# Optimization experiments

Hardware: AMD Instinct MI355X
Metric: run time of the kernel (lower is better)

The kernel has to match this reference:

```python
import jax, jax.numpy as jnp
import numpy as np
from jax import lax

T, IN_DIM, H = 8192, 512, 1024


def setup_inputs() -> dict:
    key = jax.random.key(0)
    ks = jax.random.split(key, 6)
    def lin(k, fan_in, shape):
        return jax.random.normal(k, shape, dtype=jnp.float32) / np.sqrt(fan_in)
    return {
        "x": jax.random.normal(ks[0], (T, IN_DIM), dtype=jnp.float32),
        "W_ih_0": lin(ks[1], IN_DIM, (IN_DIM, 4 * H)),
        "W_hh_0": lin(ks[2], H, (H, 4 * H)),
        "b_0": jnp.zeros((4 * H,), dtype=jnp.float32),
        "W_ih_1": lin(ks[3], H, (H, 4 * H)),
        "W_hh_1": lin(ks[4], H, (H, 4 * H)),
        "b_1": jnp.zeros((4 * H,), dtype=jnp.float32),
    }


def _lstm_layer(inp, W_ih, W_hh, b):
    """inp: (T, D) -> hiddens (T, H). Input projection batched across all T."""
    hdim = W_hh.shape[0]
    xg = inp @ W_ih  # (T, 4H), all-timestep GEMM

    def step(carry, xg_t):
        h, c = carry
        gates = xg_t + h @ W_hh + b  # (4H,)
        i, f, g, o = jnp.split(gates, 4, axis=-1)
        i = jax.nn.sigmoid(i)
        f = jax.nn.sigmoid(f)
        g = jnp.tanh(g)
        o = jax.nn.sigmoid(o)
        new_c = f * c + i * g
        new_h = o * jnp.tanh(new_c)
        return (new_h, new_c), new_h

    init = (jnp.zeros((hdim,), inp.dtype), jnp.zeros((hdim,), inp.dtype))
    _, hiddens = lax.scan(step, init, xg)
    return hiddens  # (T, H)


def reference(x, W_ih_0, W_hh_0, b_0, W_ih_1, W_hh_1, b_1):
    h1 = _lstm_layer(x, W_ih_0, W_hh_0, b_0)
    h2 = _lstm_layer(h1, W_ih_1, W_hh_1, b_1)
    return h2
```

## Files before the change

### kernel.cpp

```cpp
#include <hip/hip_runtime.h>
#include <stdint.h>


#define TT    8192
#define INDIM 512
#define HH    1024
#define G4    4096
#define NBLK  256

#define SENT 0x7FC00000u

typedef float f32x4 __attribute__((ext_vector_type(4)));

__device__ __forceinline__ float sigf(float x) { return 1.0f / (1.0f + __expf(-x)); }

__global__ void fill4_kernel(float* __restrict__ p, long n4, uint32_t pat) {
  float pv = __uint_as_float(pat);
  f32x4 v = { pv, pv, pv, pv };
  long i = (long)blockIdx.x * blockDim.x + threadIdx.x;
  long stride = (long)gridDim.x * blockDim.x;
  for (; i < n4; i += stride) {
    const float* a = p + i * 4;
    asm volatile("global_store_dwordx4 %0, %1, off sc0 sc1" :: "v"(a), "v"(v) : "memory");
  }
}

__global__ __launch_bounds__(256, 2) void gemm_bias_f32(
    const float* __restrict__ A, const float* __restrict__ B,
    const float* __restrict__ bias, float* __restrict__ C,
    int M, int N, int K)
{
  constexpr int BM = 128, BN = 128, BK = 16, TM = 8, TN = 8;
  __shared__ float As[BK][BM];
  __shared__ float Bs[BK][BN];
  const int tid = threadIdx.x;
  const int bm = blockIdx.y * BM;
  const int bn = blockIdx.x * BN;
  const int tm = (tid >> 4) * TM;
  const int tn = (tid & 15) * TN;
  float acc[TM][TN] = {};
  for (int k0 = 0; k0 < K; k0 += BK) {
    #pragma unroll
    for (int i = 0; i < 2; ++i) {
      int idx = tid * 2 + i;
      int r = idx >> 2, c4 = idx & 3;
      float4 a = *(const float4*)(A + (size_t)(bm + r) * K + k0 + c4 * 4);
      As[c4 * 4 + 0][r] = a.x;
      As[c4 * 4 + 1][r] = a.y;
      As[c4 * 4 + 2][r] = a.z;
      As[c4 * 4 + 3][r] = a.w;
    }
    #pragma unroll
    for (int i = 0; i < 2; ++i) {
      int idx = tid * 2 + i;
      int r = idx >> 5, c4 = idx & 31;
      *(float4*)&Bs[r][c4 * 4] = *(const float4*)(B + (size_t)(k0 + r) * N + bn + c4 * 4);
    }
    __syncthreads();
    #pragma unroll
    for (int kk = 0; kk < BK; ++kk) {
      float ar[TM], br[TN];
      *(float4*)&ar[0] = *(const float4*)&As[kk][tm];
      *(float4*)&ar[4] = *(const float4*)&As[kk][tm + 4];
      *(float4*)&br[0] = *(const float4*)&Bs[kk][tn];
      *(float4*)&br[4] = *(const float4*)&Bs[kk][tn + 4];
      #pragma unroll
      for (int i = 0; i < TM; ++i)
        #pragma unroll
        for (int j = 0; j < TN; ++j)
          acc[i][j] = fmaf(ar[i], br[j], acc[i][j]);
    }
    __syncthreads();
  }
  #pragma unroll
  for (int i = 0; i < TM; ++i) {
    float* crow = C + (size_t)(bm + tm + i) * N + bn + tn;
    #pragma unroll
    for (int j = 0; j < TN; j += 4) {
      float4 v;
      v.x = acc[i][j + 0] + bias[bn + tn + j + 0];
      v.y = acc[i][j + 1] + bias[bn + tn + j + 1];
      v.z = acc[i][j + 2] + bias[bn + tn + j + 2];
      v.w = acc[i][j + 3] + bias[bn + tn + j + 3];
      *(float4*)(crow + j) = v;
    }
  }
}

__global__ __launch_bounds__(256, 1) void lstm_scan_kernel(
    const float* __restrict__ xg,
    const float* __restrict__ Whh,
    float* __restrict__ hout,
    int nsteps)
{
  __shared__ float hsh[HH];
  const int tid = threadIdx.x;
  const int w = tid >> 6;
  const int l = tid & 63;
  const int g = l >> 4;
  const int p = l & 15;
  const int u = blockIdx.x * 4 + w;
  const int col = g * HH + u;

  float wr[64];
  #pragma unroll
  for (int k = 0; k < 16; ++k)
    #pragma unroll
    for (int e = 0; e < 4; ++e)
      wr[4 * k + e] = Whh[(size_t)(4 * (p + 16 * k) + e) * G4 + col];

  float c = 0.0f;
  float xgv = xg[col];
  uint32_t budget = (1u << 20);

  for (int t = 0; t < nsteps; ++t) {
    float xg_cur = xgv;
    int tnx = (t + 1 < nsteps) ? t + 1 : t;
    xgv = xg[(size_t)tnx * G4 + col];

    float red = 0.0f;
    if (t > 0) {
      const float* ha = hout + (size_t)(t - 1) * HH + tid * 4;
      f32x4 hvv;
      int hd = 0;
      do {
        asm volatile("global_load_dwordx4 %0, %1, off sc0 sc1"
                     : "=v"(hvv) : "v"(ha));
        asm volatile("s_waitcnt vmcnt(0)" ::: "memory");
        __builtin_amdgcn_sched_barrier(0);
        hd = (__float_as_uint(hvv.x) != SENT) & (__float_as_uint(hvv.y) != SENT)
           & (__float_as_uint(hvv.z) != SENT) & (__float_as_uint(hvv.w) != SENT);
        if (!hd) --budget;
      } while (!hd && budget);
      if (!hd) {
        if (__float_as_uint(hvv.x) == SENT) hvv.x = 0.0f;
        if (__float_as_uint(hvv.y) == SENT) hvv.y = 0.0f;
        if (__float_as_uint(hvv.z) == SENT) hvv.z = 0.0f;
        if (__float_as_uint(hvv.w) == SENT) hvv.w = 0.0f;
      }
      __syncthreads();
      *(f32x4*)&hsh[tid * 4] = hvv;
      __syncthreads();

      float s0 = 0.f, s1 = 0.f, s2 = 0.f, s3 = 0.f;
      #pragma unroll
      for (int k = 0; k < 16; ++k) {
        f32x4 hk = *(const f32x4*)&hsh[p * 4 + 64 * k];
        s0 = fmaf(wr[4 * k + 0], hk.x, s0);
        s1 = fmaf(wr[4 * k + 1], hk.y, s1);
        s2 = fmaf(wr[4 * k + 2], hk.z, s2);
        s3 = fmaf(wr[4 * k + 3], hk.w, s3);
      }
      red = (s0 + s1) + (s2 + s3);
      #pragma unroll
      for (int m = 1; m < 16; m <<= 1) red += __shfl_xor(red, m, 64);
    }

    float gp = red + xg_cur;
    float gi_ = __shfl(gp, 0, 64);
    float gf_ = __shfl(gp, 16, 64);
    float gg_ = __shfl(gp, 32, 64);
    float go_ = __shfl(gp, 48, 64);
    float iv = sigf(gi_);
    float fv = sigf(gf_);
    float gv = tanhf(gg_);
    float ov = sigf(go_);
    c = fv * c + iv * gv;
    float h = ov * tanhf(c);
    if (l == 0) {
      __hip_atomic_store(hout + (size_t)t * HH + u, h,
                         __ATOMIC_RELAXED, __HIP_MEMORY_SCOPE_SYSTEM);
    }
  }
}

extern "C" void kernel_launch(void* const* d_in, const int* in_sizes, int n_in,
                              void* d_out, int out_size, void* d_ws, size_t ws_size,
                              hipStream_t stream)
{
  const float* x    = (const float*)d_in[0];
  const float* Wih0 = (const float*)d_in[1];
  const float* Whh0 = (const float*)d_in[2];
  const float* b0   = (const float*)d_in[3];
  const float* Wih1 = (const float*)d_in[4];
  const float* Whh1 = (const float*)d_in[5];
  const float* b1   = (const float*)d_in[6];
  float* out = (float*)d_out;

  float* ws    = (float*)d_ws;
  float* xgbuf = ws;
  float* h1    = ws + (size_t)TT * G4;

  fill4_kernel<<<2048, 256, 0, stream>>>(h1, (long)TT * HH / 4, SENT);
  fill4_kernel<<<2048, 256, 0, stream>>>(out, (long)TT * HH / 4, SENT);

  dim3 gblk(256);
  dim3 ggrid(G4 / 128, TT / 128);

  gemm_bias_f32<<<ggrid, gblk, 0, stream>>>(x, Wih0, b0, xgbuf, TT, G4, INDIM);
  lstm_scan_kernel<<<NBLK, 256, 0, stream>>>(xgbuf, Whh0, h1, TT);
  gemm_bias_f32<<<ggrid, gblk, 0, stream>>>(h1, Wih1, b1, xgbuf, TT, G4, HH);
  lstm_scan_kernel<<<NBLK, 256, 0, stream>>>(xgbuf, Whh1, out, TT);
}
```

Baseline: 38.65 ms.

## Fuse both LSTM layers into one wavefront-pipelined persistent kernel

Launches a single kernel of 512 blocks. The first 256 run the layer-0 recurrence and the other 256 run layer 1, which spin-waits on each layer-0 hidden state and computes its input projection inline from register-resident W_ih1 weights. This removes the second full GEMM and lets the two sequential scans overlap in time, so total latency moves toward one scan length. It relies on all 512 blocks being co-resident (launch bounds set to 2 per CU) to avoid deadlock, doubles the per-step dot work for layer 1, and replaces tanhf with a clamped exp-based approximation.

```diff
diff --git a/kernel.cpp b/kernel.cpp
--- a/kernel.cpp
+++ b/kernel.cpp
@@ -13,6 +13,11 @@
 typedef float f32x4 __attribute__((ext_vector_type(4)));
 
 __device__ __forceinline__ float sigf(float x) { return 1.0f / (1.0f + __expf(-x)); }
+__device__ __forceinline__ float tanhfast(float x) {
+  x = fminf(fmaxf(x, -20.0f), 20.0f);
+  float e = __expf(2.0f * x);
+  return (e - 1.0f) / (e + 1.0f);
+}
 
 __global__ void fill4_kernel(float* __restrict__ p, long n4, uint32_t pat) {
   float pv = __uint_as_float(pat);
@@ -87,89 +92,189 @@
   }
 }
 
-__global__ __launch_bounds__(256, 1) void lstm_scan_kernel(
+__global__ __launch_bounds__(256, 2) void lstm_fused_kernel(
     const float* __restrict__ xg,
-    const float* __restrict__ Whh,
-    float* __restrict__ hout,
+    const float* __restrict__ Whh0,
+    const float* __restrict__ Wih1,
+    const float* __restrict__ Whh1,
+    const float* __restrict__ b1,
+    float* __restrict__ h1buf,
+    float* __restrict__ h2buf,
     int nsteps)
 {
-  __shared__ float hsh[HH];
+  __shared__ float sh1[HH];
+  __shared__ float sh2[HH];
   const int tid = threadIdx.x;
   const int w = tid >> 6;
   const int l = tid & 63;
   const int g = l >> 4;
   const int p = l & 15;
-  const int u = blockIdx.x * 4 + w;
+  const int lay = blockIdx.x >> 8;
+  const int bid = blockIdx.x & 255;
+  const int u = bid * 4 + w;
   const int col = g * HH + u;
 
-  float wr[64];
-  #pragma unroll
-  for (int k = 0; k < 16; ++k)
-    #pragma unroll
-    for (int e = 0; e < 4; ++e)
-      wr[4 * k + e] = Whh[(size_t)(4 * (p + 16 * k) + e) * G4 + col];
-
+  uint32_t budget = (1u << 20);
   float c = 0.0f;
-  float xgv = xg[col];
-  uint32_t budget = (1u << 20);
-
-  for (int t = 0; t < nsteps; ++t) {
-    float xg_cur = xgv;
-    int tnx = (t + 1 < nsteps) ? t + 1 : t;
-    xgv = xg[(size_t)tnx * G4 + col];
-
-    float red = 0.0f;
-    if (t > 0) {
-      const float* ha = hout + (size_t)(t - 1) * HH + tid * 4;
-      f32x4 hvv;
+
+  if (lay == 0) {
+    float wr[64];
+    #pragma unroll
+    for (int k = 0; k < 16; ++k)
+      #pragma unroll
+      for (int e = 0; e < 4; ++e)
+        wr[4 * k + e] = Whh0[(size_t)(4 * (p + 16 * k) + e) * G4 + col];
+
+    float xgv = xg[col];
+    for (int t = 0; t < nsteps; ++t) {
+      float xg_cur = xgv;
+      int tnx = (t + 1 < nsteps) ? t + 1 : t;
+      xgv = xg[(size_t)tnx * G4 + col];
+
+      float red = 0.0f;
+      if (t > 0) {
+        const float* ha = h1buf + (size_t)(t - 1) * HH + tid * 4;
+        f32x4 hvv;
+        int hd = 0;
+        do {
+          asm volatile("global_load_dwordx4 %0, %1, off sc0 sc1"
+                       : "=v"(hvv) : "v"(ha));
+          asm volatile("s_waitcnt vmcnt(0)" ::: "memory");
+          __builtin_amdgcn_sched_barrier(0);
+          hd = (__float_as_uint(hvv.x) != SENT) & (__float_as_uint(hvv.y) != SENT)
+             & (__float_as_uint(hvv.z) != SENT) & (__float_as_uint(hvv.w) != SENT);
+          if (!hd) --budget;
+        } while (!hd && budget);
+        if (!hd) {
+          if (__float_as_uint(hvv.x) == SENT) hvv.x = 0.0f;
+          if (__float_as_uint(hvv.y) == SENT) hvv.y = 0.0f;
+          if (__float_as_uint(hvv.z) == SENT) hvv.z = 0.0f;
+          if (__float_as_uint(hvv.w) == SENT) hvv.w = 0.0f;
+        }
+        __syncthreads();
+        *(f32x4*)&sh1[tid * 4] = hvv;
+        __syncthreads();
+
+        float s0 = 0.f, s1 = 0.f, s2 = 0.f, s3 = 0.f;
+        #pragma unroll
+        for (int k = 0; k < 16; ++k) {
+          f32x4 hk = *(const f32x4*)&sh1[p * 4 + 64 * k];
+          s0 = fmaf(wr[4 * k + 0], hk.x, s0);
+          s1 = fmaf(wr[4 * k + 1], hk.y, s1);
+          s2 = fmaf(wr[4 * k + 2], hk.z, s2);
+          s3 = fmaf(wr[4 * k + 3], hk.w, s3);
+        }
+        red = (s0 + s1) + (s2 + s3);
+        #pragma unroll
+        for (int m = 1; m < 16; m <<= 1) red += __shfl_xor(red, m, 64);
+      }
+
+      float gp = red + xg_cur;
+      float gi_ = __shfl(gp, 0, 64);
+      float gf_ = __shfl(gp, 16, 64);
+      float gg_ = __shfl(gp, 32, 64);
+      float go_ = __shfl(gp, 48, 64);
+      float iv = sigf(gi_);
+      float fv = sigf(gf_);
+      float gv = tanhfast(gg_);
+      float ov = sigf(go_);
+      c = fv * c + iv * gv;
+      float h = ov * tanhfast(c);
+      if (l == 0) {
+        __hip_atomic_store(h1buf + (size_t)t * HH + u, h,
+                           __ATOMIC_RELAXED, __HIP_MEMORY_SCOPE_SYSTEM);
+      }
+    }
+  } else {
+    float wr_hh[64], wr_ih[64];
+    #pragma unroll
+    for (int k = 0; k < 16; ++k)
+      #pragma unroll
+      for (int e = 0; e < 4; ++e) {
+        size_t row = (size_t)(4 * (p + 16 * k) + e);
+        wr_hh[4 * k + e] = Whh1[row * G4 + col];
+        wr_ih[4 * k + e] = Wih1[row * G4 + col];
+      }
+    const float bv = b1[col];
+
+    for (int t = 0; t < nsteps; ++t) {
+      const float* ha1 = h1buf + (size_t)t * HH + tid * 4;
+      const float* ha2 = h2buf + (size_t)(t - 1) * HH + tid * 4;
+      f32x4 v1, v2;
       int hd = 0;
-      do {
-        asm volatile("global_load_dwordx4 %0, %1, off sc0 sc1"
-                     : "=v"(hvv) : "v"(ha));
-        asm volatile("s_waitcnt vmcnt(0)" ::: "memory");
-        __builtin_amdgcn_sched_barrier(0);
-        hd = (__float_as_uint(hvv.x) != SENT) & (__float_as_uint(hvv.y) != SENT)
-           & (__float_as_uint(hvv.z) != SENT) & (__float_as_uint(hvv.w) != SENT);
-        if (!hd) --budget;
-      } while (!hd && budget);
+      if (t > 0) {
+        do {
+          asm volatile("global_load_dwordx4 %0, %2, off sc0 sc1\n\t"
+                       "global_load_dwordx4 %1, %3, off sc0 sc1"
+                       : "=v"(v1), "=v"(v2) : "v"(ha1), "v"(ha2));
+          asm volatile("s_waitcnt vmcnt(0)" ::: "memory");
+          __builtin_amdgcn_sched_barrier(0);
+          hd = (__float_as_uint(v1.x) != SENT) & (__float_as_uint(v1.y) != SENT)
+             & (__float_as_uint(v1.z) != SENT) & (__float_as_uint(v1.w) != SENT)
+             & (__float_as_uint(v2.x) != SENT) & (__float_as_uint(v2.y) != SENT)
+             & (__float_as_uint(v2.z) != SENT) & (__float_as_uint(v2.w) != SENT);
+          if (!hd) --budget;
+        } while (!hd && budget);
+      } else {
+        do {
+          asm volatile("global_load_dwordx4 %0, %1, off sc0 sc1"
+                       : "=v"(v1) : "v"(ha1));
+          asm volatile("s_waitcnt vmcnt(0)" ::: "memory");
+          __builtin_amdgcn_sched_barrier(0);
+          hd = (__float_as_uint(v1.x) != SENT) & (__float_as_uint(v1.y) != SENT)
+             & (__float_as_uint(v1.z) != SENT) & (__float_as_uint(v1.w) != SENT);
+          if (!hd) --budget;
+        } while (!hd && budget);
+        v2 = f32x4{0.f, 0.f, 0.f, 0.f};
+      }
       if (!hd) {
-        if (__float_as_uint(hvv.x) == SENT) hvv.x = 0.0f;
-        if (__float_as_uint(hvv.y) == SENT) hvv.y = 0.0f;
-        if (__float_as_uint(hvv.z) == SENT) hvv.z = 0.0f;
-        if (__float_as_uint(hvv.w) == SENT) hvv.w = 0.0f;
+        if (__float_as_uint(v1.x) == SENT) v1.x = 0.0f;
+        if (__float_as_uint(v1.y) == SENT) v1.y = 0.0f;
+        if (__float_as_uint(v1.z) == SENT) v1.z = 0.0f;
+        if (__float_as_uint(v1.w) == SENT) v1.w = 0.0f;
+        if (__float_as_uint(v2.x) == SENT) v2.x = 0.0f;
+        if (__float_as_uint(v2.y) == SENT) v2.y = 0.0f;
+        if (__float_as_uint(v2.z) == SENT) v2.z = 0.0f;
+        if (__float_as_uint(v2.w) == SENT) v2.w = 0.0f;
       }
       __syncthreads();
-      *(f32x4*)&hsh[tid * 4] = hvv;
+      *(f32x4*)&sh1[tid * 4] = v1;
+      *(f32x4*)&sh2[tid * 4] = v2;
       __syncthreads();
 
       float s0 = 0.f, s1 = 0.f, s2 = 0.f, s3 = 0.f;
       #pragma unroll
       for (int k = 0; k < 16; ++k) {
-        f32x4 hk = *(const f32x4*)&hsh[p * 4 + 64 * k];
-        s0 = fmaf(wr[4 * k + 0], hk.x, s0);
-        s1 = fmaf(wr[4 * k + 1], hk.y, s1);
-        s2 = fmaf(wr[4 * k + 2], hk.z, s2);
-        s3 = fmaf(wr[4 * k + 3], hk.w, s3);
-      }
-      red = (s0 + s1) + (s2 + s3);
+        f32x4 a = *(const f32x4*)&sh1[p * 4 + 64 * k];
+        f32x4 b = *(const f32x4*)&sh2[p * 4 + 64 * k];
+        s0 = fmaf(wr_ih[4 * k + 0], a.x, s0);
+        s1 = fmaf(wr_ih[4 * k + 1], a.y, s1);
+        s2 = fmaf(wr_ih[4 * k + 2], a.z, s2);
+        s3 = fmaf(wr_ih[4 * k + 3], a.w, s3);
+        s0 = fmaf(wr_hh[4 * k + 0], b.x, s0);
+        s1 = fmaf(wr_hh[4 * k + 1], b.y, s1);
+        s2 = fmaf(wr_hh[4 * k + 2], b.z, s2);
+        s3 = fmaf(wr_hh[4 * k + 3], b.w, s3);
+      }
+      float red = (s0 + s1) + (s2 + s3);
       #pragma unroll
       for (int m = 1; m < 16; m <<= 1) red += __shfl_xor(red, m, 64);
-    }
-
-    float gp = red + xg_cur;
-    float gi_ = __shfl(gp, 0, 64);
-    float gf_ = __shfl(gp, 16, 64);
-    float gg_ = __shfl(gp, 32, 64);
-    float go_ = __shfl(gp, 48, 64);
-    float iv = sigf(gi_);
-    float fv = sigf(gf_);
-    float gv = tanhf(gg_);
-    float ov = sigf(go_);
-    c = fv * c + iv * gv;
-    float h = ov * tanhf(c);
-    if (l == 0) {
-      __hip_atomic_store(hout + (size_t)t * HH + u, h,
-                         __ATOMIC_RELAXED, __HIP_MEMORY_SCOPE_SYSTEM);
+
+      float gp = red + bv;
+      float gi_ = __shfl(gp, 0, 64);
+      float gf_ = __shfl(gp, 16, 64);
+      float gg_ = __shfl(gp, 32, 64);
+      float go_ = __shfl(gp, 48, 64);
+      float iv = sigf(gi_);
+      float fv = sigf(gf_);
+      float gv = tanhfast(gg_);
+      float ov = sigf(go_);
+      c = fv * c + iv * gv;
+      float h = ov * tanhfast(c);
+      if (l == 0) {
+        __hip_atomic_store(h2buf + (size_t)t * HH + u, h,
+                           __ATOMIC_RELAXED, __HIP_MEMORY_SCOPE_SYSTEM);
+      }
     }
   }
 }
@@ -198,7 +303,6 @@
   dim3 ggrid(G4 / 128, TT / 128);
 
   gemm_bias_f32<<<ggrid, gblk, 0, stream>>>(x, Wih0, b0, xgbuf, TT, G4, INDIM);
-  lstm_scan_kernel<<<NBLK, 256, 0, stream>>>(xgbuf, Whh0, h1, TT);
-  gemm_bias_f32<<<ggrid, gblk, 0, stream>>>(h1, Wih1, b1, xgbuf, TT, G4, HH);
-  lstm_scan_kernel<<<NBLK, 256, 0, stream>>>(xgbuf, Whh1, out, TT);
-}
+  lstm_fused_kernel<<<2 * NBLK, 256, 0, stream>>>(
+      xgbuf, Whh0, Wih1, Whh1, b1, h1, out, TT);
+}
```

Measured after the change: 37.30 ms. -3.5%, faster.
